# Kernel optimization log

Hardware: AMD Instinct MI355X
Metric: run time of the kernel (lower is better)

## Reference

```python
import jax, jax.numpy as jnp
import numpy as np

B, T, IN, H, N, W, R, NW, OUT = 16, 64, 256, 512, 256, 64, 4, 1, 256
NM = 1 + 2 * NW  # read modes
EPS = 1e-6

# interface slice offsets
_sizes = [R*W, R, NW*W, NW, NW*W, NW*W, R, NW, NW, R*NM]
_offs = np.concatenate([[0], np.cumsum(_sizes)])

def _oneplus(x):
    return 1.0 + jax.nn.softplus(x)

def _content_weights(M, keys, strengths):
    # M: [B,N,W], keys: [B,h,W], strengths: [B,h] -> [B,h,N]
    Mn = M / (jnp.linalg.norm(M, axis=-1, keepdims=True) + EPS)
    kn = keys / (jnp.linalg.norm(keys, axis=-1, keepdims=True) + EPS)
    sim = jnp.einsum('bnw,bhw->bhn', Mn, kn)
    return jax.nn.softmax(_oneplus(strengths)[..., None] * sim, axis=-1)

def setup_inputs() -> dict:
    key = jax.random.key(0)
    ks = jax.random.split(key, 5)
    s = 0.02
    return {
        'inputs': jax.random.normal(ks[0], (T, B, IN), jnp.float32),
        'W_ih': jax.random.normal(ks[1], (4*H, IN + R*W), jnp.float32) * s,
        'W_hh': jax.random.normal(ks[2], (4*H, H), jnp.float32) * s,
        'b_ih': jnp.zeros((4*H,), jnp.float32),
        'b_hh': jnp.zeros((4*H,), jnp.float32),
        'W_int': jax.random.normal(ks[3], (H, int(_offs[-1])), jnp.float32) * s,
        'b_int': jnp.zeros((int(_offs[-1]),), jnp.float32),
        'W_out': jax.random.normal(ks[4], (OUT, H + R*W), jnp.float32) * s,
        'b_out': jnp.zeros((OUT,), jnp.float32),
    }

def _dnc_forward(inputs, W_ih, W_hh, b_ih, b_hh, W_int, b_int, W_out, b_out):
    off_diag = 1.0 - jnp.eye(N, dtype=inputs.dtype)

    def step(carry, x_t):
        h, c, M, usage, link, prec, wr, ww_prev, read_words = carry
        ctrl_in = jnp.concatenate([x_t, read_words.reshape(B, -1)], axis=1)
        gates = ctrl_in @ W_ih.T + h @ W_hh.T + (b_ih + b_hh)
        i, f, g, o = jnp.split(gates, 4, axis=1)  # torch LSTM gate order
        c = jax.nn.sigmoid(f) * c + jax.nn.sigmoid(i) * jnp.tanh(g)
        h = jax.nn.sigmoid(o) * jnp.tanh(c)

        itf = h @ W_int + b_int
        def sl(j, shape):
            return itf[:, _offs[j]:_offs[j+1]].reshape((B,) + shape)
        read_keys = sl(0, (R, W)); read_str = sl(1, (R,))
        write_keys = sl(2, (NW, W)); write_str = sl(3, (NW,))
        erase = jax.nn.sigmoid(sl(4, (NW, W)))
        write_vec = jax.nn.sigmoid(sl(5, (NW, W)))
        free_gate = jax.nn.sigmoid(sl(6, (R,)))
        alloc_gate = jax.nn.sigmoid(sl(7, (NW,)))
        write_gate = jax.nn.sigmoid(sl(8, (NW,)))
        modes = jax.nn.softmax(sl(9, (R, NM)), axis=2)

        # usage with previous write weights and free gates over previous reads
        psi = jnp.prod(1.0 - free_gate[:, :, None] * wr, axis=1)  # [B,N]
        ww_agg = 1.0 - jnp.prod(1.0 - ww_prev, axis=1)
        usage = (usage + ww_agg - usage * ww_agg) * psi

        # allocation weighting (sort ascending usage)
        idx = jnp.argsort(usage, axis=1)
        u_s = jnp.take_along_axis(usage, idx, axis=1)
        prod_excl = jnp.cumprod(jnp.concatenate([jnp.ones((B, 1), usage.dtype), u_s[:, :-1]], axis=1), axis=1)
        a_s = (1.0 - u_s) * prod_excl
        alloc = jnp.zeros_like(usage).at[jnp.arange(B)[:, None], idx].set(a_s)

        cw = _content_weights(M, write_keys, write_str)  # [B,NW,N]
        ww = write_gate[..., None] * (alloc_gate[..., None] * alloc[:, None, :] + (1.0 - alloc_gate[..., None]) * cw)

        # memory erase + write
        M = M * jnp.prod(1.0 - ww[:, :, :, None] * erase[:, :, None, :], axis=1)
        M = M + jnp.einsum('bhn,bhw->bnw', ww, write_vec)

        # temporal link update (uses old precedence)
        ww_i = ww[..., :, None]; ww_j = ww[..., None, :]
        link = (1.0 - ww_i - ww_j) * link + ww_i * prec[:, :, None, :]
        link = link * off_diag
        prec = (1.0 - ww.sum(-1, keepdims=True)) * prec + ww

        fwd = jnp.einsum('bwij,brj->brwi', link, wr)
        bwd = jnp.einsum('bwji,brj->brwi', link, wr)
        cr = _content_weights(M, read_keys, read_str)  # [B,R,N]
        mb, mf, mc = modes[..., :NW], modes[..., NW:2*NW], modes[..., 2*NW]
        wr = jnp.einsum('brw,brwn->brn', mb, bwd) + jnp.einsum('brw,brwn->brn', mf, fwd) + mc[..., None] * cr
        read_words = jnp.einsum('brn,bnw->brw', wr, M)

        pre = jnp.concatenate([h, read_words.reshape(B, -1)], axis=1)
        out = pre @ W_out.T + b_out
        return (h, c, M, usage, link, prec, wr, ww, read_words), out

    z = jnp.zeros
    dt = inputs.dtype
    carry0 = (z((B, H), dt), z((B, H), dt), z((B, N, W), dt), z((B, N), dt),
              z((B, NW, N, N), dt), z((B, NW, N), dt), z((B, R, N), dt),
              z((B, NW, N), dt), z((B, R, W), dt))
    _, outs = jax.lax.scan(step, carry0, inputs)
    return outs  # [T,B,OUT]

def reference(inputs, W_ih, W_hh, b_ih, b_hh, W_int, b_int, W_out, b_out):
    return _dnc_forward(inputs, W_ih, W_hh, b_ih, b_hh, W_int, b_int, W_out, b_out)
```

## Files before the change

kernel.cpp:

```cpp
#include <hip/hip_runtime.h>
#include <math.h>

#define BT 256

#define Bx 16
#define Tt 64
#define INx 256

__device__ __forceinline__ float sigm(float v) { return 1.0f / (1.0f + expf(-v)); }
__device__ __forceinline__ float oneplusf(float v) { return 1.0f + ((v > 15.0f) ? v : log1pf(expf(v))); }
__device__ __forceinline__ float4 ld4(const float* p) { return *reinterpret_cast<const float4*>(p); }

#define ZERO_FLOATS 1376256

__global__ __launch_bounds__(BT) void k_zero(float* __restrict__ ws) {
    int g = blockIdx.x * BT + threadIdx.x;
    for (int i = g; i < ZERO_FLOATS; i += gridDim.x * BT) ws[i] = 0.0f;
}

__global__ __launch_bounds__(BT)
void k_gates(const float* __restrict__ x,
             const float* __restrict__ W_ih, const float* __restrict__ W_hh,
             const float* __restrict__ b_ih, const float* __restrict__ b_hh,
             const float* __restrict__ W_out, const float* __restrict__ b_out,
             const float* __restrict__ hr, float* __restrict__ hw,
             float* __restrict__ cst, const float* __restrict__ rwb,
             const float* __restrict__ oh, float* __restrict__ out, int t)
{
    const int bl = blockIdx.x, tid = threadIdx.x;
    __shared__ float red[1024];
    if (bl < 128) {
        int pl = tid >> 2, ks = tid & 3;
        int p = bl * 64 + pl;
        int b = p & 15, j = p >> 4;
        float a0 = 0, a1 = 0, a2 = 0, a3 = 0;
        const float *src, *w0, *w1, *w2, *w3;
        if (ks < 2) {
            int kofs = ks * 256;
            src = (ks == 0) ? (x + (t * Bx + b) * INx) : (rwb + b * 256);
            w0 = W_ih + (j)        * 512 + kofs;
            w1 = W_ih + (j + 512)  * 512 + kofs;
            w2 = W_ih + (j + 1024) * 512 + kofs;
            w3 = W_ih + (j + 1536) * 512 + kofs;
        } else {
            int kofs = (ks - 2) * 256;
            src = hr + b * 512 + kofs;
            w0 = W_hh + (j)        * 512 + kofs;
            w1 = W_hh + (j + 512)  * 512 + kofs;
            w2 = W_hh + (j + 1024) * 512 + kofs;
            w3 = W_hh + (j + 1536) * 512 + kofs;
        }
        for (int kk = 0; kk < 256; kk += 4) {
            float4 iv = ld4(src + kk);
            float4 q0 = ld4(w0 + kk);
            a0 += iv.x * q0.x + iv.y * q0.y + iv.z * q0.z + iv.w * q0.w;
            float4 q1 = ld4(w1 + kk);
            a1 += iv.x * q1.x + iv.y * q1.y + iv.z * q1.z + iv.w * q1.w;
            float4 q2 = ld4(w2 + kk);
            a2 += iv.x * q2.x + iv.y * q2.y + iv.z * q2.z + iv.w * q2.w;
            float4 q3 = ld4(w3 + kk);
            a3 += iv.x * q3.x + iv.y * q3.y + iv.z * q3.z + iv.w * q3.w;
        }
        red[pl * 16 + 0 * 4 + ks] = a0;
        red[pl * 16 + 1 * 4 + ks] = a1;
        red[pl * 16 + 2 * 4 + ks] = a2;
        red[pl * 16 + 3 * 4 + ks] = a3;
        __syncthreads();
        if (ks == 0) {
            const float* rp = red + pl * 16;
            float gi = rp[0]  + rp[1]  + rp[2]  + rp[3]  + b_ih[j]        + b_hh[j];
            float gf = rp[4]  + rp[5]  + rp[6]  + rp[7]  + b_ih[j + 512]  + b_hh[j + 512];
            float gg = rp[8]  + rp[9]  + rp[10] + rp[11] + b_ih[j + 1024] + b_hh[j + 1024];
            float go = rp[12] + rp[13] + rp[14] + rp[15] + b_ih[j + 1536] + b_hh[j + 1536];
            float cv = cst[b * 512 + j];
            cv = sigm(gf) * cv + sigm(gi) * tanhf(gg);
            float hv = sigm(go) * tanhf(cv);
            cst[b * 512 + j] = cv;
            hw[b * 512 + j] = hv;
        }
    } else if (t > 0) {
        int b = bl - 128, o = tid;
        float acc = b_out[o];
        acc += oh[b * 256 + o] + oh[(16 + b) * 256 + o] + oh[(32 + b) * 256 + o] + oh[(48 + b) * 256 + o];
        const float* wrow = W_out + o * 768 + 512;
        const float* rwp = rwb + b * 256;
        for (int k = 0; k < 256; k += 4) {
            float4 w4 = ld4(wrow + k);
            acc += rwp[k] * w4.x + rwp[k + 1] * w4.y + rwp[k + 2] * w4.z + rwp[k + 3] * w4.w;
        }
        out[((t - 1) * Bx + b) * 256 + o] = acc;
    }
}

__global__ __launch_bounds__(BT)
void k_itf(const float* __restrict__ hw, const float* __restrict__ W_int,
           const float* __restrict__ b_int, float* __restrict__ itf,
           const float* __restrict__ W_out, float* __restrict__ oh)
{
    const int bl = blockIdx.x, tid = threadIdx.x;
    __shared__ float red[4096];
    if (bl < 15) {
        int jl = tid & 31, ks = tid >> 5;
        int j = bl * 32 + jl;
        float acc[16];
#pragma unroll
        for (int b = 0; b < 16; b++) acc[b] = 0.f;
        if (j < 471) {
            for (int k = ks * 64; k < ks * 64 + 64; ++k) {
                float wv = W_int[k * 471 + j];
#pragma unroll
                for (int b = 0; b < 16; b++) acc[b] += hw[b * 512 + k] * wv;
            }
        }
#pragma unroll
        for (int b = 0; b < 16; b++) red[tid * 16 + b] = acc[b];
        __syncthreads();
        int jl2 = tid & 31, bh = tid >> 5;
        int j2 = bl * 32 + jl2;
        for (int rep = 0; rep < 2; ++rep) {
            int b2 = bh + 8 * rep;
            if (j2 < 471) {
                float s = 0;
#pragma unroll
                for (int ksx = 0; ksx < 8; ksx++) s += red[(ksx * 32 + jl2) * 16 + b2];
                itf[b2 * 471 + j2] = s + b_int[j2];
            }
        }
    } else {
        int idx = bl - 15;
        int b = idx >> 2, ks = idx & 3;
        int o = tid;
        const float* wrow = W_out + o * 768 + ks * 128;
        const float* hb = hw + b * 512 + ks * 128;
        float acc = 0;
        for (int k = 0; k < 128; k += 4) {
            float4 w4 = ld4(wrow + k);
            acc += hb[k] * w4.x + hb[k + 1] * w4.y + hb[k + 2] * w4.z + hb[k + 3] * w4.w;
        }
        oh[(ks * 16 + b) * 256 + o] = acc;
    }
}

__global__ __launch_bounds__(BT)
void k_iface(const float* __restrict__ itf, const float* __restrict__ Mb,
             const float* __restrict__ nrm, float* __restrict__ usg,
             const float* __restrict__ wrb, float* __restrict__ wwb,
             const float* __restrict__ pr_r, float* __restrict__ pr_w,
             float* __restrict__ ers, float* __restrict__ wvs,
             float* __restrict__ rso, float* __restrict__ mds)
{
    const int b = blockIdx.x, tid = threadIdx.x;
    __shared__ float smem[1152];
    __shared__ int s_idx[256];
    float* s_keys = smem;
    float* s_cw   = smem + 256;
    float* s_al   = smem + 512;
    float* s_tmp  = smem + 768;
    float* s_wk   = smem + 1024;
    float* s_sc   = smem + 1088;
    const float* it = itf + b * 471;

    if (tid < 4) {
        float m0 = it[459 + tid * 3], m1 = it[460 + tid * 3], m2 = it[461 + tid * 3];
        float mx3 = fmaxf(m0, fmaxf(m1, m2));
        float e0 = expf(m0 - mx3), e1 = expf(m1 - mx3), e2 = expf(m2 - mx3);
        float inv = 1.f / (e0 + e1 + e2);
        mds[(b * 4 + tid) * 3 + 0] = e0 * inv;
        mds[(b * 4 + tid) * 3 + 1] = e1 * inv;
        mds[(b * 4 + tid) * 3 + 2] = e2 * inv;
        rso[b * 4 + tid] = oneplusf(it[256 + tid]);
        s_sc[tid] = sigm(it[453 + tid]);
    }
    if (tid == 4) s_sc[4] = sigm(it[457]);
    if (tid == 5) s_sc[5] = sigm(it[458]);
    if (tid == 6) s_sc[6] = oneplusf(it[324]);
    if (tid < 64) {
        ers[b * 64 + tid] = sigm(it[325 + tid]);
        wvs[b * 64 + tid] = sigm(it[389 + tid]);
        s_wk[tid] = it[260 + tid];
    }
    __syncthreads();
    if (tid < 64) {
        float v = s_wk[tid] * s_wk[tid];
        for (int o2 = 32; o2 > 0; o2 >>= 1) v += __shfl_down(v, o2);
        if (tid == 0) s_sc[7] = sqrtf(v);
    }
    __syncthreads();
    {
        int n = tid;
        float psi = 1.f;
#pragma unroll
        for (int r = 0; r < 4; r++) psi *= (1.f - s_sc[r] * wrb[b * 1024 + r * 256 + n]);
        float wwp = wwb[b * 256 + n];
        float u = usg[b * 256 + n];
        u = (u + wwp - u * wwp) * psi;
        usg[b * 256 + n] = u;
        s_keys[n] = u;
        s_idx[n] = n;
        const float* Mr = Mb + (b * 256 + n) * 64;
        float dot = 0;
        for (int w = 0; w < 64; w += 4) {
            float4 m4 = ld4(Mr + w);
            dot += m4.x * s_wk[w] + m4.y * s_wk[w + 1] + m4.z * s_wk[w + 2] + m4.w * s_wk[w + 3];
        }
        s_cw[n] = s_sc[6] * dot / ((nrm[b * 256 + n] + 1e-6f) * (s_sc[7] + 1e-6f));
    }
    __syncthreads();
    s_tmp[tid] = s_cw[tid];
    __syncthreads();
    for (int s2 = 128; s2 > 0; s2 >>= 1) { if (tid < s2) s_tmp[tid] = fmaxf(s_tmp[tid], s_tmp[tid + s2]); __syncthreads(); }
    float mx = s_tmp[0];
    __syncthreads();
    float ex = expf(s_cw[tid] - mx);
    s_tmp[tid] = ex;
    __syncthreads();
    for (int s2 = 128; s2 > 0; s2 >>= 1) { if (tid < s2) s_tmp[tid] += s_tmp[tid + s2]; __syncthreads(); }
    float cwv = ex / s_tmp[0];
    __syncthreads();
    s_cw[tid] = cwv;
    for (int kk2 = 2; kk2 <= 256; kk2 <<= 1) {
        for (int j2 = kk2 >> 1; j2 > 0; j2 >>= 1) {
            int ixj = tid ^ j2;
            if (ixj > tid) {
                float ka = s_keys[tid], kb = s_keys[ixj];
                int ia = s_idx[tid], ib = s_idx[ixj];
                bool up = ((tid & kk2) == 0);
                bool sw = up ? (kb < ka || (kb == ka && ib < ia))
                             : (ka < kb || (ka == kb && ia < ib));
                if (sw) { s_keys[tid] = kb; s_keys[ixj] = ka; s_idx[tid] = ib; s_idx[ixj] = ia; }
            }
            __syncthreads();
        }
    }
    s_tmp[tid] = s_keys[tid];
    __syncthreads();
    for (int o2 = 1; o2 < 256; o2 <<= 1) {
        float pv = (tid >= o2) ? s_tmp[tid - o2] : 1.0f;
        __syncthreads();
        s_tmp[tid] *= pv;
        __syncthreads();
    }
    float excl = (tid == 0) ? 1.0f : s_tmp[tid - 1];
    float a_s = (1.0f - s_keys[tid]) * excl;
    s_al[s_idx[tid]] = a_s;
    __syncthreads();
    float ag = s_sc[4], wg = s_sc[5];
    float wwn = wg * (ag * s_al[tid] + (1.f - ag) * s_cw[tid]);
    wwb[b * 256 + tid] = wwn;
    s_tmp[tid] = wwn;
    __syncthreads();
    for (int s2 = 128; s2 > 0; s2 >>= 1) { if (tid < s2) s_tmp[tid] += s_tmp[tid + s2]; __syncthreads(); }
    float S = s_tmp[0];
    pr_w[b * 256 + tid] = (1.f - S) * pr_r[b * 256 + tid] + wwn;
}

__global__ __launch_bounds__(BT)
void k_linkmem(const float* __restrict__ wwb, const float* __restrict__ pr_r,
               float* __restrict__ lnk, const float* __restrict__ wrb,
               float* __restrict__ bwp, float* __restrict__ Mb,
               const float* __restrict__ ers, const float* __restrict__ wvs,
               float* __restrict__ nrm)
{
    const int bl = blockIdx.x, tid = threadIdx.x;
    if (bl < 128) {
        int b = bl >> 3, ch = bl & 7;
        int ci = tid;
        float wwc = wwb[b * 256 + ci];
        float pco = pr_r[b * 256 + ci];
        float* Lb = lnk + b * 65536;
        float b0 = 0, b1 = 0, b2 = 0, b3 = 0;
        int r0 = ch * 32;
        for (int rr = 0; rr < 32; ++rr) {
            int ri = r0 + rr;
            float wwr = wwb[b * 256 + ri];
            float v = Lb[ri * 256 + ci];
            v = (1.f - wwr - wwc) * v + wwr * pco;
            if (ci == ri) v = 0.f;
            Lb[ri * 256 + ci] = v;
            b0 += v * wrb[b * 1024 + ri];
            b1 += v * wrb[b * 1024 + 256 + ri];
            b2 += v * wrb[b * 1024 + 512 + ri];
            b3 += v * wrb[b * 1024 + 768 + ri];
        }
        float* bp = bwp + ((b * 8 + ch) * 4) * 256;
        bp[ci] = b0; bp[256 + ci] = b1; bp[512 + ci] = b2; bp[768 + ci] = b3;
    } else {
        int b = bl - 128;
        int w = tid & 63, rg = tid >> 6;
        float er = ers[b * 64 + w], wv = wvs[b * 64 + w];
        for (int it2 = 0; it2 < 64; ++it2) {
            int n = rg + 4 * it2;
            float wwn = wwb[b * 256 + n];
            float m = Mb[(b * 256 + n) * 64 + w];
            m = m * (1.f - wwn * er) + wwn * wv;
            Mb[(b * 256 + n) * 64 + w] = m;
            float s = m * m;
            for (int o2 = 32; o2 > 0; o2 >>= 1) s += __shfl_down(s, o2);
            if (w == 0) nrm[b * 256 + n] = sqrtf(s);
        }
    }
}

__global__ __launch_bounds__(BT)
void k_read(const float* __restrict__ lnk, const float* __restrict__ bwp,
            const float* __restrict__ Mb, const float* __restrict__ nrm,
            const float* __restrict__ itf, const float* __restrict__ rso,
            const float* __restrict__ mds, float* __restrict__ wrb,
            float* __restrict__ rwb)
{
    const int bl = blockIdx.x, tid = threadIdx.x;
    __shared__ float smem[896];
    int b = bl >> 2, r = bl & 3;
    float* s_wr  = smem;
    float* s_tmp = smem + 512;
    float* s_key = smem + 768;
    float* s_sc  = smem + 840;
    s_wr[tid] = wrb[b * 1024 + r * 256 + tid];
    if (tid < 64) s_key[tid] = itf[b * 471 + r * 64 + tid];
    __syncthreads();
    if (tid < 64) {
        float v = s_key[tid] * s_key[tid];
        for (int o2 = 32; o2 > 0; o2 >>= 1) v += __shfl_down(v, o2);
        if (tid == 0) s_sc[0] = sqrtf(v);
    }
    __syncthreads();
    int n = tid;
    const float* bp = bwp + b * 8192 + r * 256 + n;
    float bwd_n = 0;
#pragma unroll
    for (int ch = 0; ch < 8; ++ch) bwd_n += bp[ch * 1024];
    const float* Lr = lnk + b * 65536 + n * 256;
    float fwd_n = 0;
    for (int j2 = 0; j2 < 256; j2 += 4) {
        float4 l4 = ld4(Lr + j2);
        fwd_n += l4.x * s_wr[j2] + l4.y * s_wr[j2 + 1] + l4.z * s_wr[j2 + 2] + l4.w * s_wr[j2 + 3];
    }
    const float* Mr = Mb + (b * 256 + n) * 64;
    float dot = 0;
    for (int w = 0; w < 64; w += 4) {
        float4 m4 = ld4(Mr + w);
        dot += m4.x * s_key[w] + m4.y * s_key[w + 1] + m4.z * s_key[w + 2] + m4.w * s_key[w + 3];
    }
    float simv = rso[b * 4 + r] * dot / ((nrm[b * 256 + n] + 1e-6f) * (s_sc[0] + 1e-6f));
    s_tmp[tid] = simv;
    __syncthreads();
    for (int s2 = 128; s2 > 0; s2 >>= 1) { if (tid < s2) s_tmp[tid] = fmaxf(s_tmp[tid], s_tmp[tid + s2]); __syncthreads(); }
    float mx = s_tmp[0];
    __syncthreads();
    float ex = expf(simv - mx);
    s_tmp[tid] = ex;
    __syncthreads();
    for (int s2 = 128; s2 > 0; s2 >>= 1) { if (tid < s2) s_tmp[tid] += s_tmp[tid + s2]; __syncthreads(); }
    float crv = ex / s_tmp[0];
    float mbv = mds[(b * 4 + r) * 3 + 0];
    float mfv = mds[(b * 4 + r) * 3 + 1];
    float mcv = mds[(b * 4 + r) * 3 + 2];
    float wrn = mbv * bwd_n + mfv * fwd_n + mcv * crv;
    wrb[b * 1024 + r * 256 + n] = wrn;
    __syncthreads();
    s_wr[tid] = wrn;
    __syncthreads();
    int w = tid & 63, gq = tid >> 6;
    float p = 0;
    const float* Mg = Mb + b * 256 * 64;
    for (int n2 = gq * 64; n2 < gq * 64 + 64; ++n2)
        p += s_wr[n2] * Mg[n2 * 64 + w];
    s_tmp[tid] = p;
    __syncthreads();
    if (tid < 64)
        rwb[b * 256 + r * 64 + tid] = s_tmp[tid] + s_tmp[tid + 64] + s_tmp[tid + 128] + s_tmp[tid + 192];
}

__global__ __launch_bounds__(BT)
void k_final(const float* __restrict__ oh, const float* __restrict__ W_out,
             const float* __restrict__ b_out, const float* __restrict__ rwb,
             float* __restrict__ out)
{
    int b = blockIdx.x, o = threadIdx.x;
    float acc = b_out[o];
    acc += oh[b * 256 + o] + oh[(16 + b) * 256 + o] + oh[(32 + b) * 256 + o] + oh[(48 + b) * 256 + o];
    const float* wrow = W_out + o * 768 + 512;
    const float* rwp = rwb + b * 256;
    for (int k = 0; k < 256; k += 4) {
        float4 w4 = ld4(wrow + k);
        acc += rwp[k] * w4.x + rwp[k + 1] * w4.y + rwp[k + 2] * w4.z + rwp[k + 3] * w4.w;
    }
    out[((Tt - 1) * Bx + b) * 256 + o] = acc;
}

extern "C" void kernel_launch(void* const* d_in, const int* in_sizes, int n_in,
                              void* d_out, int out_size, void* d_ws, size_t ws_size,
                              hipStream_t stream) {
    const float* x     = (const float*)d_in[0];
    const float* W_ih  = (const float*)d_in[1];
    const float* W_hh  = (const float*)d_in[2];
    const float* b_ih  = (const float*)d_in[3];
    const float* b_hh  = (const float*)d_in[4];
    const float* W_int = (const float*)d_in[5];
    const float* b_int = (const float*)d_in[6];
    const float* W_out = (const float*)d_in[7];
    const float* b_out = (const float*)d_in[8];
    float* outp = (float*)d_out;
    float* ws   = (float*)d_ws;

    float* h0  = ws + 0;
    float* h1  = ws + 8192;
    float* cst = ws + 16384;
    float* Mb  = ws + 24576;
    float* usg = ws + 286720;
    float* lnk = ws + 290816;
    float* pr0 = ws + 1339392;
    float* pr1 = ws + 1343488;
    float* wrb = ws + 1347584;
    float* wwb = ws + 1363968;
    float* rwb = ws + 1368064;
    float* nrm = ws + 1372160;
    float* itf = ws + 1376256;
    float* ers = ws + 1383792;
    float* wvs = ws + 1384816;
    float* rso = ws + 1385840;
    float* mds = ws + 1385904;
    float* oh  = ws + 1386096;
    float* bwp = ws + 1402480;
    (void)usg;

    k_zero<<<672, BT, 0, stream>>>(ws);
    for (int t = 0; t < Tt; ++t) {
        const float* hr = (t & 1) ? h1 : h0;
        float*       hw = (t & 1) ? h0 : h1;
        const float* pr_r = (t & 1) ? pr1 : pr0;
        float*       pr_w = (t & 1) ? pr0 : pr1;
        k_gates<<<144, BT, 0, stream>>>(x, W_ih, W_hh, b_ih, b_hh, W_out, b_out,
                                        hr, hw, cst, rwb, oh, outp, t);
        k_itf<<<79, BT, 0, stream>>>(hw, W_int, b_int, itf, W_out, oh);
        k_iface<<<16, BT, 0, stream>>>(itf, Mb, nrm, ws + 286720, wrb, wwb,
                                       pr_r, pr_w, ers, wvs, rso, mds);
        k_linkmem<<<144, BT, 0, stream>>>(wwb, pr_r, lnk, wrb, bwp, Mb, ers, wvs, nrm);
        k_read<<<64, BT, 0, stream>>>(lnk, bwp, Mb, nrm, itf, rso, mds, wrb, rwb);
    }
    k_final<<<16, BT, 0, stream>>>(oh, W_out, b_out, rwb, outp);
}
```

Baseline: 9.310 ms.

## Fuse per-step kernels into one persistent kernel with global barriers

Replaces the five launches per timestep (over 320 in total) with a single persistent kernel of 144 blocks. Phases are separated by a software grid barrier built on atomics. The change also replaces the bitonic sort in the allocation step with a rank-by-counting scheme and moves the W_out hidden projection into the interface phase. It removes launch overhead and inter-kernel gaps, at the cost of spin-wait barriers that rely on all 144 blocks being co-resident.

Measured after the change: 23.04 ms. 2.47x slower.

```diff
diff --git a/kernel.cpp b/kernel.cpp
--- a/kernel.cpp
+++ b/kernel.cpp
@@ -1,6 +1,7 @@
 #include <hip/hip_runtime.h>
 #include <math.h>
 
+#define NB 144
 #define BT 256
 
 #define Bx 16
@@ -11,397 +12,38 @@
 __device__ __forceinline__ float oneplusf(float v) { return 1.0f + ((v > 15.0f) ? v : log1pf(expf(v))); }
 __device__ __forceinline__ float4 ld4(const float* p) { return *reinterpret_cast<const float4*>(p); }
 
-#define ZERO_FLOATS 1376256
-
-__global__ __launch_bounds__(BT) void k_zero(float* __restrict__ ws) {
-    int g = blockIdx.x * BT + threadIdx.x;
-    for (int i = g; i < ZERO_FLOATS; i += gridDim.x * BT) ws[i] = 0.0f;
-}
-
-__global__ __launch_bounds__(BT)
-void k_gates(const float* __restrict__ x,
-             const float* __restrict__ W_ih, const float* __restrict__ W_hh,
-             const float* __restrict__ b_ih, const float* __restrict__ b_hh,
-             const float* __restrict__ W_out, const float* __restrict__ b_out,
-             const float* __restrict__ hr, float* __restrict__ hw,
-             float* __restrict__ cst, const float* __restrict__ rwb,
-             const float* __restrict__ oh, float* __restrict__ out, int t)
-{
-    const int bl = blockIdx.x, tid = threadIdx.x;
-    __shared__ float red[1024];
-    if (bl < 128) {
-        int pl = tid >> 2, ks = tid & 3;
-        int p = bl * 64 + pl;
-        int b = p & 15, j = p >> 4;
-        float a0 = 0, a1 = 0, a2 = 0, a3 = 0;
-        const float *src, *w0, *w1, *w2, *w3;
-        if (ks < 2) {
-            int kofs = ks * 256;
-            src = (ks == 0) ? (x + (t * Bx + b) * INx) : (rwb + b * 256);
-            w0 = W_ih + (j)        * 512 + kofs;
-            w1 = W_ih + (j + 512)  * 512 + kofs;
-            w2 = W_ih + (j + 1024) * 512 + kofs;
-            w3 = W_ih + (j + 1536) * 512 + kofs;
+__device__ int g_cnt = 0;
+__device__ int g_gen = 0;
+
+__device__ __forceinline__ void gbar() {
+    __syncthreads();
+    if (threadIdx.x == 0) {
+        int g = __hip_atomic_load(&g_gen, __ATOMIC_RELAXED, __HIP_MEMORY_SCOPE_AGENT);
+        int a = __hip_atomic_fetch_add(&g_cnt, 1, __ATOMIC_ACQ_REL, __HIP_MEMORY_SCOPE_AGENT);
+        if (a == NB - 1) {
+            __hip_atomic_store(&g_cnt, 0, __ATOMIC_RELAXED, __HIP_MEMORY_SCOPE_AGENT);
+            __hip_atomic_store(&g_gen, g + 1, __ATOMIC_RELEASE, __HIP_MEMORY_SCOPE_AGENT);
         } else {
-            int kofs = (ks - 2) * 256;
-            src = hr + b * 512 + kofs;
-            w0 = W_hh + (j)        * 512 + kofs;
-            w1 = W_hh + (j + 512)  * 512 + kofs;
-            w2 = W_hh + (j + 1024) * 512 + kofs;
-            w3 = W_hh + (j + 1536) * 512 + kofs;
-        }
-        for (int kk = 0; kk < 256; kk += 4) {
-            float4 iv = ld4(src + kk);
-            float4 q0 = ld4(w0 + kk);
-            a0 += iv.x * q0.x + iv.y * q0.y + iv.z * q0.z + iv.w * q0.w;
-            float4 q1 = ld4(w1 + kk);
-            a1 += iv.x * q1.x + iv.y * q1.y + iv.z * q1.z + iv.w * q1.w;
-            float4 q2 = ld4(w2 + kk);
-            a2 += iv.x * q2.x + iv.y * q2.y + iv.z * q2.z + iv.w * q2.w;
-            float4 q3 = ld4(w3 + kk);
-            a3 += iv.x * q3.x + iv.y * q3.y + iv.z * q3.z + iv.w * q3.w;
-        }
-        red[pl * 16 + 0 * 4 + ks] = a0;
-        red[pl * 16 + 1 * 4 + ks] = a1;
-        red[pl * 16 + 2 * 4 + ks] = a2;
-        red[pl * 16 + 3 * 4 + ks] = a3;
-        __syncthreads();
-        if (ks == 0) {
-            const float* rp = red + pl * 16;
-            float gi = rp[0]  + rp[1]  + rp[2]  + rp[3]  + b_ih[j]        + b_hh[j];
-            float gf = rp[4]  + rp[5]  + rp[6]  + rp[7]  + b_ih[j + 512]  + b_hh[j + 512];
-            float gg = rp[8]  + rp[9]  + rp[10] + rp[11] + b_ih[j + 1024] + b_hh[j + 1024];
-            float go = rp[12] + rp[13] + rp[14] + rp[15] + b_ih[j + 1536] + b_hh[j + 1536];
-            float cv = cst[b * 512 + j];
-            cv = sigm(gf) * cv + sigm(gi) * tanhf(gg);
-            float hv = sigm(go) * tanhf(cv);
-            cst[b * 512 + j] = cv;
-            hw[b * 512 + j] = hv;
-        }
-    } else if (t > 0) {
-        int b = bl - 128, o = tid;
-        float acc = b_out[o];
-        acc += oh[b * 256 + o] + oh[(16 + b) * 256 + o] + oh[(32 + b) * 256 + o] + oh[(48 + b) * 256 + o];
-        const float* wrow = W_out + o * 768 + 512;
-        const float* rwp = rwb + b * 256;
-        for (int k = 0; k < 256; k += 4) {
-            float4 w4 = ld4(wrow + k);
-            acc += rwp[k] * w4.x + rwp[k + 1] * w4.y + rwp[k + 2] * w4.z + rwp[k + 3] * w4.w;
-        }
-        out[((t - 1) * Bx + b) * 256 + o] = acc;
-    }
-}
-
-__global__ __launch_bounds__(BT)
-void k_itf(const float* __restrict__ hw, const float* __restrict__ W_int,
-           const float* __restrict__ b_int, float* __restrict__ itf,
-           const float* __restrict__ W_out, float* __restrict__ oh)
-{
-    const int bl = blockIdx.x, tid = threadIdx.x;
-    __shared__ float red[4096];
-    if (bl < 15) {
-        int jl = tid & 31, ks = tid >> 5;
-        int j = bl * 32 + jl;
-        float acc[16];
-#pragma unroll
-        for (int b = 0; b < 16; b++) acc[b] = 0.f;
-        if (j < 471) {
-            for (int k = ks * 64; k < ks * 64 + 64; ++k) {
-                float wv = W_int[k * 471 + j];
-#pragma unroll
-                for (int b = 0; b < 16; b++) acc[b] += hw[b * 512 + k] * wv;
-            }
-        }
-#pragma unroll
-        for (int b = 0; b < 16; b++) red[tid * 16 + b] = acc[b];
-        __syncthreads();
-        int jl2 = tid & 31, bh = tid >> 5;
-        int j2 = bl * 32 + jl2;
-        for (int rep = 0; rep < 2; ++rep) {
-            int b2 = bh + 8 * rep;
-            if (j2 < 471) {
-                float s = 0;
-#pragma unroll
-                for (int ksx = 0; ksx < 8; ksx++) s += red[(ksx * 32 + jl2) * 16 + b2];
-                itf[b2 * 471 + j2] = s + b_int[j2];
-            }
-        }
-    } else {
-        int idx = bl - 15;
-        int b = idx >> 2, ks = idx & 3;
-        int o = tid;
-        const float* wrow = W_out + o * 768 + ks * 128;
-        const float* hb = hw + b * 512 + ks * 128;
-        float acc = 0;
-        for (int k = 0; k < 128; k += 4) {
-            float4 w4 = ld4(wrow + k);
-            acc += hb[k] * w4.x + hb[k + 1] * w4.y + hb[k + 2] * w4.z + hb[k + 3] * w4.w;
-        }
-        oh[(ks * 16 + b) * 256 + o] = acc;
-    }
-}
-
-__global__ __launch_bounds__(BT)
-void k_iface(const float* __restrict__ itf, const float* __restrict__ Mb,
-             const float* __restrict__ nrm, float* __restrict__ usg,
-             const float* __restrict__ wrb, float* __restrict__ wwb,
-             const float* __restrict__ pr_r, float* __restrict__ pr_w,
-             float* __restrict__ ers, float* __restrict__ wvs,
-             float* __restrict__ rso, float* __restrict__ mds)
-{
-    const int b = blockIdx.x, tid = threadIdx.x;
-    __shared__ float smem[1152];
-    __shared__ int s_idx[256];
-    float* s_keys = smem;
-    float* s_cw   = smem + 256;
-    float* s_al   = smem + 512;
-    float* s_tmp  = smem + 768;
-    float* s_wk   = smem + 1024;
-    float* s_sc   = smem + 1088;
-    const float* it = itf + b * 471;
-
-    if (tid < 4) {
-        float m0 = it[459 + tid * 3], m1 = it[460 + tid * 3], m2 = it[461 + tid * 3];
-        float mx3 = fmaxf(m0, fmaxf(m1, m2));
-        float e0 = expf(m0 - mx3), e1 = expf(m1 - mx3), e2 = expf(m2 - mx3);
-        float inv = 1.f / (e0 + e1 + e2);
-        mds[(b * 4 + tid) * 3 + 0] = e0 * inv;
-        mds[(b * 4 + tid) * 3 + 1] = e1 * inv;
-        mds[(b * 4 + tid) * 3 + 2] = e2 * inv;
-        rso[b * 4 + tid] = oneplusf(it[256 + tid]);
-        s_sc[tid] = sigm(it[453 + tid]);
-    }
-    if (tid == 4) s_sc[4] = sigm(it[457]);
-    if (tid == 5) s_sc[5] = sigm(it[458]);
-    if (tid == 6) s_sc[6] = oneplusf(it[324]);
-    if (tid < 64) {
-        ers[b * 64 + tid] = sigm(it[325 + tid]);
-        wvs[b * 64 + tid] = sigm(it[389 + tid]);
-        s_wk[tid] = it[260 + tid];
+            while (__hip_atomic_load(&g_gen, __ATOMIC_ACQUIRE, __HIP_MEMORY_SCOPE_AGENT) == g) { }
+        }
     }
     __syncthreads();
-    if (tid < 64) {
-        float v = s_wk[tid] * s_wk[tid];
-        for (int o2 = 32; o2 > 0; o2 >>= 1) v += __shfl_down(v, o2);
-        if (tid == 0) s_sc[7] = sqrtf(v);
-    }
-    __syncthreads();
-    {
-        int n = tid;
-        float psi = 1.f;
-#pragma unroll
-        for (int r = 0; r < 4; r++) psi *= (1.f - s_sc[r] * wrb[b * 1024 + r * 256 + n]);
-        float wwp = wwb[b * 256 + n];
-        float u = usg[b * 256 + n];
-        u = (u + wwp - u * wwp) * psi;
-        usg[b * 256 + n] = u;
-        s_keys[n] = u;
-        s_idx[n] = n;
-        const float* Mr = Mb + (b * 256 + n) * 64;
-        float dot = 0;
-        for (int w = 0; w < 64; w += 4) {
-            float4 m4 = ld4(Mr + w);
-            dot += m4.x * s_wk[w] + m4.y * s_wk[w + 1] + m4.z * s_wk[w + 2] + m4.w * s_wk[w + 3];
-        }
-        s_cw[n] = s_sc[6] * dot / ((nrm[b * 256 + n] + 1e-6f) * (s_sc[7] + 1e-6f));
-    }
-    __syncthreads();
-    s_tmp[tid] = s_cw[tid];
-    __syncthreads();
-    for (int s2 = 128; s2 > 0; s2 >>= 1) { if (tid < s2) s_tmp[tid] = fmaxf(s_tmp[tid], s_tmp[tid + s2]); __syncthreads(); }
-    float mx = s_tmp[0];
-    __syncthreads();
-    float ex = expf(s_cw[tid] - mx);
-    s_tmp[tid] = ex;
-    __syncthreads();
-    for (int s2 = 128; s2 > 0; s2 >>= 1) { if (tid < s2) s_tmp[tid] += s_tmp[tid + s2]; __syncthreads(); }
-    float cwv = ex / s_tmp[0];
-    __syncthreads();
-    s_cw[tid] = cwv;
-    for (int kk2 = 2; kk2 <= 256; kk2 <<= 1) {
-        for (int j2 = kk2 >> 1; j2 > 0; j2 >>= 1) {
-            int ixj = tid ^ j2;
-            if (ixj > tid) {
-                float ka = s_keys[tid], kb = s_keys[ixj];
-                int ia = s_idx[tid], ib = s_idx[ixj];
-                bool up = ((tid & kk2) == 0);
-                bool sw = up ? (kb < ka || (kb == ka && ib < ia))
-                             : (ka < kb || (ka == kb && ia < ib));
-                if (sw) { s_keys[tid] = kb; s_keys[ixj] = ka; s_idx[tid] = ib; s_idx[ixj] = ia; }
-            }
-            __syncthreads();
-        }
-    }
-    s_tmp[tid] = s_keys[tid];
-    __syncthreads();
-    for (int o2 = 1; o2 < 256; o2 <<= 1) {
-        float pv = (tid >= o2) ? s_tmp[tid - o2] : 1.0f;
-        __syncthreads();
-        s_tmp[tid] *= pv;
-        __syncthreads();
-    }
-    float excl = (tid == 0) ? 1.0f : s_tmp[tid - 1];
-    float a_s = (1.0f - s_keys[tid]) * excl;
-    s_al[s_idx[tid]] = a_s;
-    __syncthreads();
-    float ag = s_sc[4], wg = s_sc[5];
-    float wwn = wg * (ag * s_al[tid] + (1.f - ag) * s_cw[tid]);
-    wwb[b * 256 + tid] = wwn;
-    s_tmp[tid] = wwn;
-    __syncthreads();
-    for (int s2 = 128; s2 > 0; s2 >>= 1) { if (tid < s2) s_tmp[tid] += s_tmp[tid + s2]; __syncthreads(); }
-    float S = s_tmp[0];
-    pr_w[b * 256 + tid] = (1.f - S) * pr_r[b * 256 + tid] + wwn;
 }
 
+#define ZERO_FLOATS 1376256
+
 __global__ __launch_bounds__(BT)
-void k_linkmem(const float* __restrict__ wwb, const float* __restrict__ pr_r,
-               float* __restrict__ lnk, const float* __restrict__ wrb,
-               float* __restrict__ bwp, float* __restrict__ Mb,
-               const float* __restrict__ ers, const float* __restrict__ wvs,
-               float* __restrict__ nrm)
+void dnc_persist(const float* __restrict__ x,
+                 const float* __restrict__ W_ih, const float* __restrict__ W_hh,
+                 const float* __restrict__ b_ih, const float* __restrict__ b_hh,
+                 const float* __restrict__ W_int, const float* __restrict__ b_int,
+                 const float* __restrict__ W_out, const float* __restrict__ b_out,
+                 float* out, float* ws)
 {
-    const int bl = blockIdx.x, tid = threadIdx.x;
-    if (bl < 128) {
-        int b = bl >> 3, ch = bl & 7;
-        int ci = tid;
-        float wwc = wwb[b * 256 + ci];
-        float pco = pr_r[b * 256 + ci];
-        float* Lb = lnk + b * 65536;
-        float b0 = 0, b1 = 0, b2 = 0, b3 = 0;
-        int r0 = ch * 32;
-        for (int rr = 0; rr < 32; ++rr) {
-            int ri = r0 + rr;
-            float wwr = wwb[b * 256 + ri];
-            float v = Lb[ri * 256 + ci];
-            v = (1.f - wwr - wwc) * v + wwr * pco;
-            if (ci == ri) v = 0.f;
-            Lb[ri * 256 + ci] = v;
-            b0 += v * wrb[b * 1024 + ri];
-            b1 += v * wrb[b * 1024 + 256 + ri];
-            b2 += v * wrb[b * 1024 + 512 + ri];
-            b3 += v * wrb[b * 1024 + 768 + ri];
-        }
-        float* bp = bwp + ((b * 8 + ch) * 4) * 256;
-        bp[ci] = b0; bp[256 + ci] = b1; bp[512 + ci] = b2; bp[768 + ci] = b3;
-    } else {
-        int b = bl - 128;
-        int w = tid & 63, rg = tid >> 6;
-        float er = ers[b * 64 + w], wv = wvs[b * 64 + w];
-        for (int it2 = 0; it2 < 64; ++it2) {
-            int n = rg + 4 * it2;
-            float wwn = wwb[b * 256 + n];
-            float m = Mb[(b * 256 + n) * 64 + w];
-            m = m * (1.f - wwn * er) + wwn * wv;
-            Mb[(b * 256 + n) * 64 + w] = m;
-            float s = m * m;
-            for (int o2 = 32; o2 > 0; o2 >>= 1) s += __shfl_down(s, o2);
-            if (w == 0) nrm[b * 256 + n] = sqrtf(s);
-        }
-    }
-}
-
-__global__ __launch_bounds__(BT)
-void k_read(const float* __restrict__ lnk, const float* __restrict__ bwp,
-            const float* __restrict__ Mb, const float* __restrict__ nrm,
-            const float* __restrict__ itf, const float* __restrict__ rso,
-            const float* __restrict__ mds, float* __restrict__ wrb,
-            float* __restrict__ rwb)
-{
-    const int bl = blockIdx.x, tid = threadIdx.x;
-    __shared__ float smem[896];
-    int b = bl >> 2, r = bl & 3;
-    float* s_wr  = smem;
-    float* s_tmp = smem + 512;
-    float* s_key = smem + 768;
-    float* s_sc  = smem + 840;
-    s_wr[tid] = wrb[b * 1024 + r * 256 + tid];
-    if (tid < 64) s_key[tid] = itf[b * 471 + r * 64 + tid];
-    __syncthreads();
-    if (tid < 64) {
-        float v = s_key[tid] * s_key[tid];
-        for (int o2 = 32; o2 > 0; o2 >>= 1) v += __shfl_down(v, o2);
-        if (tid == 0) s_sc[0] = sqrtf(v);
-    }
-    __syncthreads();
-    int n = tid;
-    const float* bp = bwp + b * 8192 + r * 256 + n;
-    float bwd_n = 0;
-#pragma unroll
-    for (int ch = 0; ch < 8; ++ch) bwd_n += bp[ch * 1024];
-    const float* Lr = lnk + b * 65536 + n * 256;
-    float fwd_n = 0;
-    for (int j2 = 0; j2 < 256; j2 += 4) {
-        float4 l4 = ld4(Lr + j2);
-        fwd_n += l4.x * s_wr[j2] + l4.y * s_wr[j2 + 1] + l4.z * s_wr[j2 + 2] + l4.w * s_wr[j2 + 3];
-    }
-    const float* Mr = Mb + (b * 256 + n) * 64;
-    float dot = 0;
-    for (int w = 0; w < 64; w += 4) {
-        float4 m4 = ld4(Mr + w);
-        dot += m4.x * s_key[w] + m4.y * s_key[w + 1] + m4.z * s_key[w + 2] + m4.w * s_key[w + 3];
-    }
-    float simv = rso[b * 4 + r] * dot / ((nrm[b * 256 + n] + 1e-6f) * (s_sc[0] + 1e-6f));
-    s_tmp[tid] = simv;
-    __syncthreads();
-    for (int s2 = 128; s2 > 0; s2 >>= 1) { if (tid < s2) s_tmp[tid] = fmaxf(s_tmp[tid], s_tmp[tid + s2]); __syncthreads(); }
-    float mx = s_tmp[0];
-    __syncthreads();
-    float ex = expf(simv - mx);
-    s_tmp[tid] = ex;
-    __syncthreads();
-    for (int s2 = 128; s2 > 0; s2 >>= 1) { if (tid < s2) s_tmp[tid] += s_tmp[tid + s2]; __syncthreads(); }
-    float crv = ex / s_tmp[0];
-    float mbv = mds[(b * 4 + r) * 3 + 0];
-    float mfv = mds[(b * 4 + r) * 3 + 1];
-    float mcv = mds[(b * 4 + r) * 3 + 2];
-    float wrn = mbv * bwd_n + mfv * fwd_n + mcv * crv;
-    wrb[b * 1024 + r * 256 + n] = wrn;
-    __syncthreads();
-    s_wr[tid] = wrn;
-    __syncthreads();
-    int w = tid & 63, gq = tid >> 6;
-    float p = 0;
-    const float* Mg = Mb + b * 256 * 64;
-    for (int n2 = gq * 64; n2 < gq * 64 + 64; ++n2)
-        p += s_wr[n2] * Mg[n2 * 64 + w];
-    s_tmp[tid] = p;
-    __syncthreads();
-    if (tid < 64)
-        rwb[b * 256 + r * 64 + tid] = s_tmp[tid] + s_tmp[tid + 64] + s_tmp[tid + 128] + s_tmp[tid + 192];
-}
-
-__global__ __launch_bounds__(BT)
-void k_final(const float* __restrict__ oh, const float* __restrict__ W_out,
-             const float* __restrict__ b_out, const float* __restrict__ rwb,
-             float* __restrict__ out)
-{
-    int b = blockIdx.x, o = threadIdx.x;
-    float acc = b_out[o];
-    acc += oh[b * 256 + o] + oh[(16 + b) * 256 + o] + oh[(32 + b) * 256 + o] + oh[(48 + b) * 256 + o];
-    const float* wrow = W_out + o * 768 + 512;
-    const float* rwp = rwb + b * 256;
-    for (int k = 0; k < 256; k += 4) {
-        float4 w4 = ld4(wrow + k);
-        acc += rwp[k] * w4.x + rwp[k + 1] * w4.y + rwp[k + 2] * w4.z + rwp[k + 3] * w4.w;
-    }
-    out[((Tt - 1) * Bx + b) * 256 + o] = acc;
-}
-
-extern "C" void kernel_launch(void* const* d_in, const int* in_sizes, int n_in,
-                              void* d_out, int out_size, void* d_ws, size_t ws_size,
-                              hipStream_t stream) {
-    const float* x     = (const float*)d_in[0];
-    const float* W_ih  = (const float*)d_in[1];
-    const float* W_hh  = (const float*)d_in[2];
-    const float* b_ih  = (const float*)d_in[3];
-    const float* b_hh  = (const float*)d_in[4];
-    const float* W_int = (const float*)d_in[5];
-    const float* b_int = (const float*)d_in[6];
-    const float* W_out = (const float*)d_in[7];
-    const float* b_out = (const float*)d_in[8];
-    float* outp = (float*)d_out;
-    float* ws   = (float*)d_ws;
+    const int bl = blockIdx.x;
+    const int tid = threadIdx.x;
+
+    __shared__ float smem[2112];
 
     float* h0  = ws + 0;
     float* h1  = ws + 8192;
@@ -422,21 +64,344 @@
     float* mds = ws + 1385904;
     float* oh  = ws + 1386096;
     float* bwp = ws + 1402480;
-    (void)usg;
-
-    k_zero<<<672, BT, 0, stream>>>(ws);
+
+    {
+        int g = bl * BT + tid;
+        for (int i = g; i < ZERO_FLOATS; i += NB * BT) ws[i] = 0.0f;
+    }
+    gbar();
+
     for (int t = 0; t < Tt; ++t) {
         const float* hr = (t & 1) ? h1 : h0;
         float*       hw = (t & 1) ? h0 : h1;
         const float* pr_r = (t & 1) ? pr1 : pr0;
         float*       pr_w = (t & 1) ? pr0 : pr1;
-        k_gates<<<144, BT, 0, stream>>>(x, W_ih, W_hh, b_ih, b_hh, W_out, b_out,
-                                        hr, hw, cst, rwb, oh, outp, t);
-        k_itf<<<79, BT, 0, stream>>>(hw, W_int, b_int, itf, W_out, oh);
-        k_iface<<<16, BT, 0, stream>>>(itf, Mb, nrm, ws + 286720, wrb, wwb,
-                                       pr_r, pr_w, ers, wvs, rso, mds);
-        k_linkmem<<<144, BT, 0, stream>>>(wwb, pr_r, lnk, wrb, bwp, Mb, ers, wvs, nrm);
-        k_read<<<64, BT, 0, stream>>>(lnk, bwp, Mb, nrm, itf, rso, mds, wrb, rwb);
+
+        if (bl < 128) {
+            int pl = tid >> 2, ks = tid & 3;
+            int p = bl * 64 + pl;
+            int b = p & 15, j = p >> 4;
+            float a0 = 0, a1 = 0, a2 = 0, a3 = 0;
+            const float *src, *w0, *w1, *w2, *w3;
+            if (ks < 2) {
+                int kofs = ks * 256;
+                src = (ks == 0) ? (x + (t * Bx + b) * INx) : (rwb + b * 256);
+                w0 = W_ih + (j)        * 512 + kofs;
+                w1 = W_ih + (j + 512)  * 512 + kofs;
+                w2 = W_ih + (j + 1024) * 512 + kofs;
+                w3 = W_ih + (j + 1536) * 512 + kofs;
+            } else {
+                int kofs = (ks - 2) * 256;
+                src = hr + b * 512 + kofs;
+                w0 = W_hh + (j)        * 512 + kofs;
+                w1 = W_hh + (j + 512)  * 512 + kofs;
+                w2 = W_hh + (j + 1024) * 512 + kofs;
+                w3 = W_hh + (j + 1536) * 512 + kofs;
+            }
+            for (int kk = 0; kk < 256; kk += 4) {
+                float4 iv = ld4(src + kk);
+                float4 q0 = ld4(w0 + kk);
+                a0 += iv.x * q0.x + iv.y * q0.y + iv.z * q0.z + iv.w * q0.w;
+                float4 q1 = ld4(w1 + kk);
+                a1 += iv.x * q1.x + iv.y * q1.y + iv.z * q1.z + iv.w * q1.w;
+                float4 q2 = ld4(w2 + kk);
+                a2 += iv.x * q2.x + iv.y * q2.y + iv.z * q2.z + iv.w * q2.w;
+                float4 q3 = ld4(w3 + kk);
+                a3 += iv.x * q3.x + iv.y * q3.y + iv.z * q3.z + iv.w * q3.w;
+            }
+            float* red = smem;
+            red[pl * 16 + 0 * 4 + ks] = a0;
+            red[pl * 16 + 1 * 4 + ks] = a1;
+            red[pl * 16 + 2 * 4 + ks] = a2;
+            red[pl * 16 + 3 * 4 + ks] = a3;
+            __syncthreads();
+            if (ks == 0) {
+                const float* rp = red + pl * 16;
+                float gi = rp[0]  + rp[1]  + rp[2]  + rp[3]  + b_ih[j]        + b_hh[j];
+                float gf = rp[4]  + rp[5]  + rp[6]  + rp[7]  + b_ih[j + 512]  + b_hh[j + 512];
+                float gg = rp[8]  + rp[9]  + rp[10] + rp[11] + b_ih[j + 1024] + b_hh[j + 1024];
+                float go = rp[12] + rp[13] + rp[14] + rp[15] + b_ih[j + 1536] + b_hh[j + 1536];
+                float cv = cst[b * 512 + j];
+                cv = sigm(gf) * cv + sigm(gi) * tanhf(gg);
+                float hv = sigm(go) * tanhf(cv);
+                cst[b * 512 + j] = cv;
+                hw[b * 512 + j] = hv;
+            }
+        } else if (t > 0) {
+            int b = bl - 128, o = tid;
+            float acc = b_out[o];
+            acc += oh[b * 256 + o] + oh[(16 + b) * 256 + o] + oh[(32 + b) * 256 + o] + oh[(48 + b) * 256 + o];
+            const float* wrow = W_out + o * 768 + 512;
+            const float* rwp = rwb + b * 256;
+            for (int k = 0; k < 256; k += 4) {
+                float4 w4 = ld4(wrow + k);
+                acc += rwp[k] * w4.x + rwp[k + 1] * w4.y + rwp[k + 2] * w4.z + rwp[k + 3] * w4.w;
+            }
+            out[((t - 1) * Bx + b) * 256 + o] = acc;
+        }
+        gbar();
+
+        if (bl < 16) {
+            int b = bl;
+            float* s_keys = smem;
+            float* s_cw   = smem + 256;
+            float* s_al   = smem + 512;
+            float* s_tmp  = smem + 768;
+            float* s_wk   = smem + 1024;
+            float* s_sc   = smem + 1088;
+            float* s_itf  = smem + 1104;
+            float* s_h    = smem + 1576;
+            s_h[tid]       = hw[b * 512 + tid];
+            s_h[tid + 256] = hw[b * 512 + 256 + tid];
+            __syncthreads();
+            {
+                int j0 = tid, j1 = tid + 256;
+                bool v1 = (j1 < 471);
+                float acc0 = b_int[j0];
+                float acc1 = v1 ? b_int[j1] : 0.f;
+                for (int k = 0; k < 512; k += 4) {
+                    float ha = s_h[k], hb = s_h[k + 1], hc = s_h[k + 2], hd = s_h[k + 3];
+                    const float* r0 = W_int + (size_t)k * 471;
+                    acc0 += ha * r0[j0] + hb * r0[471 + j0] + hc * r0[942 + j0] + hd * r0[1413 + j0];
+                    if (v1) acc1 += ha * r0[j1] + hb * r0[471 + j1] + hc * r0[942 + j1] + hd * r0[1413 + j1];
+                }
+                s_itf[j0] = acc0;
+                itf[b * 471 + j0] = acc0;
+                if (v1) { s_itf[j1] = acc1; itf[b * 471 + j1] = acc1; }
+            }
+            __syncthreads();
+            const float* it = s_itf;
+            if (tid < 4) {
+                float m0 = it[459 + tid * 3], m1 = it[460 + tid * 3], m2 = it[461 + tid * 3];
+                float mx3 = fmaxf(m0, fmaxf(m1, m2));
+                float e0 = expf(m0 - mx3), e1 = expf(m1 - mx3), e2 = expf(m2 - mx3);
+                float inv = 1.f / (e0 + e1 + e2);
+                mds[(b * 4 + tid) * 3 + 0] = e0 * inv;
+                mds[(b * 4 + tid) * 3 + 1] = e1 * inv;
+                mds[(b * 4 + tid) * 3 + 2] = e2 * inv;
+                rso[b * 4 + tid] = oneplusf(it[256 + tid]);
+                s_sc[tid] = sigm(it[453 + tid]);
+            }
+            if (tid == 4) s_sc[4] = sigm(it[457]);
+            if (tid == 5) s_sc[5] = sigm(it[458]);
+            if (tid == 6) s_sc[6] = oneplusf(it[324]);
+            if (tid < 64) {
+                ers[b * 64 + tid] = sigm(it[325 + tid]);
+                wvs[b * 64 + tid] = sigm(it[389 + tid]);
+                s_wk[tid] = it[260 + tid];
+            }
+            __syncthreads();
+            if (tid < 64) {
+                float v = s_wk[tid] * s_wk[tid];
+                for (int o2 = 32; o2 > 0; o2 >>= 1) v += __shfl_down(v, o2);
+                if (tid == 0) s_sc[7] = sqrtf(v);
+            }
+            __syncthreads();
+            {
+                int n = tid;
+                float psi = 1.f;
+#pragma unroll
+                for (int r = 0; r < 4; r++) psi *= (1.f - s_sc[r] * wrb[b * 1024 + r * 256 + n]);
+                float wwp = wwb[b * 256 + n];
+                float u = usg[b * 256 + n];
+                u = (u + wwp - u * wwp) * psi;
+                usg[b * 256 + n] = u;
+                s_keys[n] = u;
+                const float* Mr = Mb + (b * 256 + n) * 64;
+                float dot = 0;
+                for (int w = 0; w < 64; w += 4) {
+                    float4 m4 = ld4(Mr + w);
+                    dot += m4.x * s_wk[w] + m4.y * s_wk[w + 1] + m4.z * s_wk[w + 2] + m4.w * s_wk[w + 3];
+                }
+                s_cw[n] = s_sc[6] * dot / ((nrm[b * 256 + n] + 1e-6f) * (s_sc[7] + 1e-6f));
+            }
+            __syncthreads();
+            s_tmp[tid] = s_cw[tid];
+            __syncthreads();
+            for (int s2 = 128; s2 > 0; s2 >>= 1) { if (tid < s2) s_tmp[tid] = fmaxf(s_tmp[tid], s_tmp[tid + s2]); __syncthreads(); }
+            float mx = s_tmp[0];
+            __syncthreads();
+            float ex = expf(s_cw[tid] - mx);
+            s_tmp[tid] = ex;
+            __syncthreads();
+            for (int s2 = 128; s2 > 0; s2 >>= 1) { if (tid < s2) s_tmp[tid] += s_tmp[tid + s2]; __syncthreads(); }
+            float cwv = ex / s_tmp[0];
+            float u_n = s_keys[tid];
+            int rank = 0;
+            for (int m = 0; m < 256; ++m) {
+                float um = s_keys[m];
+                rank += (um < u_n || (um == u_n && m < tid)) ? 1 : 0;
+            }
+            __syncthreads();
+            s_al[rank] = u_n;
+            __syncthreads();
+            s_tmp[tid] = s_al[tid];
+            __syncthreads();
+            for (int o2 = 1; o2 < 256; o2 <<= 1) {
+                float pv = (tid >= o2) ? s_tmp[tid - o2] : 1.0f;
+                __syncthreads();
+                s_tmp[tid] *= pv;
+                __syncthreads();
+            }
+            float excl = (rank == 0) ? 1.0f : s_tmp[rank - 1];
+            float a_n = (1.0f - u_n) * excl;
+            float ag = s_sc[4], wg = s_sc[5];
+            float wwn = wg * (ag * a_n + (1.f - ag) * cwv);
+            wwb[b * 256 + tid] = wwn;
+            __syncthreads();
+            s_tmp[tid] = wwn;
+            __syncthreads();
+            for (int s2 = 128; s2 > 0; s2 >>= 1) { if (tid < s2) s_tmp[tid] += s_tmp[tid + s2]; __syncthreads(); }
+            float S = s_tmp[0];
+            pr_w[b * 256 + tid] = (1.f - S) * pr_r[b * 256 + tid] + wwn;
+        } else if (bl < 80) {
+            int idx = bl - 16;
+            int b = idx >> 2, ks = idx & 3;
+            int o = tid;
+            const float* wrow = W_out + o * 768 + ks * 128;
+            const float* hb = hw + b * 512 + ks * 128;
+            float acc = 0;
+            for (int k = 0; k < 128; k += 4) {
+                float4 w4 = ld4(wrow + k);
+                acc += hb[k] * w4.x + hb[k + 1] * w4.y + hb[k + 2] * w4.z + hb[k + 3] * w4.w;
+            }
+            oh[(ks * 16 + b) * 256 + o] = acc;
+        }
+        gbar();
+
+        if (bl < 128) {
+            int b = bl >> 3, ch = bl & 7;
+            int ci = tid;
+            float wwc = wwb[b * 256 + ci];
+            float pco = pr_r[b * 256 + ci];
+            float* Lb = lnk + b * 65536;
+            float b0 = 0, b1 = 0, b2 = 0, b3 = 0;
+            int r0 = ch * 32;
+            for (int rr = 0; rr < 32; ++rr) {
+                int ri = r0 + rr;
+                float wwr = wwb[b * 256 + ri];
+                float v = Lb[ri * 256 + ci];
+                v = (1.f - wwr - wwc) * v + wwr * pco;
+                if (ci == ri) v = 0.f;
+                Lb[ri * 256 + ci] = v;
+                b0 += v * wrb[b * 1024 + ri];
+                b1 += v * wrb[b * 1024 + 256 + ri];
+                b2 += v * wrb[b * 1024 + 512 + ri];
+                b3 += v * wrb[b * 1024 + 768 + ri];
+            }
+            float* bp = bwp + ((b * 8 + ch) * 4) * 256;
+            bp[ci] = b0; bp[256 + ci] = b1; bp[512 + ci] = b2; bp[768 + ci] = b3;
+        } else {
+            int b = bl - 128;
+            int w = tid & 63, rg = tid >> 6;
+            float er = ers[b * 64 + w], wv = wvs[b * 64 + w];
+            for (int it2 = 0; it2 < 64; ++it2) {
+                int n = rg + 4 * it2;
+                float wwn = wwb[b * 256 + n];
+                float m = Mb[(b * 256 + n) * 64 + w];
+                m = m * (1.f - wwn * er) + wwn * wv;
+                Mb[(b * 256 + n) * 64 + w] = m;
+                float s = m * m;
+                for (int o2 = 32; o2 > 0; o2 >>= 1) s += __shfl_down(s, o2);
+                if (w == 0) nrm[b * 256 + n] = sqrtf(s);
+            }
+        }
+        gbar();
+
+        if (bl < 64) {
+            int b = bl >> 2, r = bl & 3;
+            float* s_wr  = smem;
+            float* s_tmp = smem + 512;
+            float* s_key = smem + 768;
+            float* s_sc  = smem + 840;
+            s_wr[tid] = wrb[b * 1024 + r * 256 + tid];
+            if (tid < 64) s_key[tid] = itf[b * 471 + r * 64 + tid];
+            __syncthreads();
+            if (tid < 64) {
+                float v = s_key[tid] * s_key[tid];
+                for (int o2 = 32; o2 > 0; o2 >>= 1) v += __shfl_down(v, o2);
+                if (tid == 0) s_sc[0] = sqrtf(v);
+            }
+            __syncthreads();
+            int n = tid;
+            const float* bp = bwp + b * 8192 + r * 256 + n;
+            float bwd_n = 0;
+#pragma unroll
+            for (int ch = 0; ch < 8; ++ch) bwd_n += bp[ch * 1024];
+            const float* Lr = lnk + b * 65536 + n * 256;
+            float fwd_n = 0;
+            for (int j2 = 0; j2 < 256; j2 += 4) {
+                float4 l4 = ld4(Lr + j2);
+                fwd_n += l4.x * s_wr[j2] + l4.y * s_wr[j2 + 1] + l4.z * s_wr[j2 + 2] + l4.w * s_wr[j2 + 3];
+            }
+            const float* Mr = Mb + (b * 256 + n) * 64;
+            float dot = 0;
+            for (int w = 0; w < 64; w += 4) {
+                float4 m4 = ld4(Mr + w);
+                dot += m4.x * s_key[w] + m4.y * s_key[w + 1] + m4.z * s_key[w + 2] + m4.w * s_key[w + 3];
+            }
+            float simv = rso[b * 4 + r] * dot / ((nrm[b * 256 + n] + 1e-6f) * (s_sc[0] + 1e-6f));
+            s_tmp[tid] = simv;
+            __syncthreads();
+            for (int s2 = 128; s2 > 0; s2 >>= 1) { if (tid < s2) s_tmp[tid] = fmaxf(s_tmp[tid], s_tmp[tid + s2]); __syncthreads(); }
+            float mx = s_tmp[0];
+            __syncthreads();
+            float ex = expf(simv - mx);
+            s_tmp[tid] = ex;
+            __syncthreads();
+            for (int s2 = 128; s2 > 0; s2 >>= 1) { if (tid < s2) s_tmp[tid] += s_tmp[tid + s2]; __syncthreads(); }
+            float crv = ex / s_tmp[0];
+            float mbv = mds[(b * 4 + r) * 3 + 0];
+            float mfv = mds[(b * 4 + r) * 3 + 1];
+            float mcv = mds[(b * 4 + r) * 3 + 2];
+            float wrn = mbv * bwd_n + mfv * fwd_n + mcv * crv;
+            wrb[b * 1024 + r * 256 + n] = wrn;
+            __syncthreads();
+            s_wr[tid] = wrn;
+            __syncthreads();
+            int w = tid & 63, gq = tid >> 6;
+            float p = 0;
+            const float* Mg = Mb + b * 256 * 64;
+            for (int n2 = gq * 64; n2 < gq * 64 + 64; ++n2)
+                p += s_wr[n2] * Mg[n2 * 64 + w];
+            s_tmp[tid] = p;
+            __syncthreads();
+            if (tid < 64)
+                rwb[b * 256 + r * 64 + tid] = s_tmp[tid] + s_tmp[tid + 64] + s_tmp[tid + 128] + s_tmp[tid + 192];
+        }
+        gbar();
     }
-    k_final<<<16, BT, 0, stream>>>(oh, W_out, b_out, rwb, outp);
+
+    if (bl >= 128) {
+        int b = bl - 128, o = tid;
+        float acc = b_out[o];
+        acc += oh[b * 256 + o] + oh[(16 + b) * 256 + o] + oh[(32 + b) * 256 + o] + oh[(48 + b) * 256 + o];
+        const float* wrow = W_out + o * 768 + 512;
+        const float* rwp = rwb + b * 256;
+        for (int k = 0; k < 256; k += 4) {
+            float4 w4 = ld4(wrow + k);
+            acc += rwp[k] * w4.x + rwp[k + 1] * w4.y + rwp[k + 2] * w4.z + rwp[k + 3] * w4.w;
+        }
+        out[((Tt - 1) * Bx + b) * 256 + o] = acc;
+    }
 }
+
+extern "C" void kernel_launch(void* const* d_in, const int* in_sizes, int n_in,
+                              void* d_out, int out_size, void* d_ws, size_t ws_size,
+                              hipStream_t stream) {
+    const float* x     = (const float*)d_in[0];
+    const float* W_ih  = (const float*)d_in[1];
+    const float* W_hh  = (const float*)d_in[2];
+    const float* b_ih  = (const float*)d_in[3];
+    const float* b_hh  = (const float*)d_in[4];
+    const float* W_int = (const float*)d_in[5];
+    const float* b_int = (const float*)d_in[6];
+    const float* W_out = (const float*)d_in[7];
+    const float* b_out = (const float*)d_in[8];
+    float* outp = (float*)d_out;
+    float* wsp  = (float*)d_ws;
+
+    dnc_persist<<<dim3(NB), dim3(BT), 0, stream>>>(x, W_ih, W_hh, b_ih, b_hh,
+                                                   W_int, b_int, W_out, b_out,
+                                                   outp, wsp);
+}
```
